# Kernel tuning notes

Measured on AMD Instinct MI355X. Metric: run time of the kernel, lower is better.

## Reference

```python
import jax, jax.numpy as jnp
import numpy as np

B, T, E, H = 8, 2048, 1024, 64

def setup_inputs() -> dict:
    key = jax.random.key(0)
    ks = jax.random.split(key, 7)
    s = 1.0 / np.sqrt(E)
    return {
        "x": jax.random.normal(ks[0], (B, T, E), dtype=jnp.float32),
        "Wq": jax.random.uniform(ks[1], (E, H), jnp.float32, -s, s),
        "bq": jax.random.uniform(ks[2], (H,), jnp.float32, -s, s),
        "Wk": jax.random.uniform(ks[3], (E, H), jnp.float32, -s, s),
        "bk": jax.random.uniform(ks[4], (H,), jnp.float32, -s, s),
        "Wv": jax.random.uniform(ks[5], (E, H), jnp.float32, -s, s),
        "bv": jax.random.uniform(ks[6], (H,), jnp.float32, -s, s),
        "mask": jnp.ones((B, T), dtype=jnp.int32),
    }

def reference(x, Wq, bq, Wk, bk, Wv, bv, mask):
    # QKV projections: [B,T,E] @ [E,H] -> [B,T,H]
    q = x @ Wq + bq
    k = x @ Wk + bk
    v = x @ Wv + bv
    scale = jnp.asarray(H, x.dtype) ** -0.5
    attn = jnp.einsum("bqh,bkh->bqk", q, k) * scale  # [B,T,T]
    pad = mask.astype(bool)[:, None, :]  # key padding mask broadcast over queries
    attn = jnp.where(pad, attn, jnp.asarray(-1e9, attn.dtype))
    attn = jax.nn.softmax(attn, axis=-1)
    # dropout p=0.0 (eval) -> identity
    return jnp.einsum("bqk,bkh->bqh", attn, v)
```

## Files before the change

### kernel.cpp

```cpp
#include <hip/hip_runtime.h>
#include <hip/hip_bf16.h>
#include <stdint.h>


typedef __attribute__((ext_vector_type(8))) short short8;
typedef __attribute__((ext_vector_type(4))) float floatx4;
typedef __attribute__((ext_vector_type(2))) uint32_t uint2v;
typedef __attribute__((ext_vector_type(4))) uint32_t uint4v;

static constexpr int Tn = 2048, En = 1024, Hn = 64;
static constexpr float kLog2e = 1.44269504088896340736f;

static __device__ __forceinline__ ushort f2bf(float f) {
  uint32_t u = __builtin_bit_cast(uint32_t, f);
  u += 0x7FFFu + ((u >> 16) & 1u);
  return (ushort)(u >> 16);
}
static __device__ __forceinline__ uint32_t cvt_pk(float lo, float hi) {
  uint32_t r;
  asm("v_cvt_pk_bf16_f32 %0, %1, %2" : "=v"(r) : "v"(lo), "v"(hi));
  return r;
}

__global__ __launch_bounds__(64) void k_packw(const float* __restrict__ Wq,
                                              const float* __restrict__ Wk,
                                              const float* __restrict__ Wv,
                                              ushort* __restrict__ wpack) {
  int blk = blockIdx.x;
  int kstep = blk / 12, ntile = blk % 12;
  int l = threadIdx.x;
  const float* W = (ntile < 4) ? Wq : (ntile < 8) ? Wk : Wv;
  int col = (ntile & 3) * 16 + (l & 15);
  int k0 = kstep * 32 + (l >> 4) * 8;
  short8 v;
#pragma unroll
  for (int j = 0; j < 8; ++j) v[j] = (short)f2bf(W[(k0 + j) * Hn + col]);
  *reinterpret_cast<short8*>(wpack + ((size_t)(kstep * 12 + ntile) * 64 + l) * 8) = v;
}

__global__ __launch_bounds__(256, 4) void k_qkv(const float* __restrict__ x,
                                                const ushort* __restrict__ wpack,
                                                const float* __restrict__ bq,
                                                const float* __restrict__ bk,
                                                const float* __restrict__ bv,
                                                ushort* __restrict__ q,
                                                ushort* __restrict__ k,
                                                ushort* __restrict__ vT2) {
  __shared__ float accS[2][64][28];
  int l = threadIdx.x & 63;
  int w = threadIdx.x >> 6;
  int ns = w & 1, ks2 = w >> 1;
  int n0 = ns * 6;
  int batch = blockIdx.x & 7;
  int chunk = blockIdx.x >> 3;
  int row0 = batch * Tn + chunk * 16;
  int lq = l & 15, g = l >> 4;
  const float* xrow = x + (size_t)(row0 + lq) * En + ks2 * 512 + g * 8;
  const ushort* wp = wpack + (size_t)l * 8;

  floatx4 acc[6];
#pragma unroll
  for (int n = 0; n < 6; ++n) acc[n] = (floatx4){0.f, 0.f, 0.f, 0.f};

  floatx4 xa[2][2];
  short8 bfr[2][6];
  xa[0][0] = *reinterpret_cast<const floatx4*>(xrow);
  xa[0][1] = *reinterpret_cast<const floatx4*>(xrow + 4);
  {
    int ks = ks2 * 16;
#pragma unroll
    for (int nn = 0; nn < 6; ++nn)
      bfr[0][nn] = *reinterpret_cast<const short8*>(wp + (size_t)(ks * 12 + n0 + nn) * 512);
  }

#pragma unroll
  for (int i = 0; i < 16; ++i) {
    const int cur = i & 1, nxt = cur ^ 1;
    if (i < 15) {
      xa[nxt][0] = *reinterpret_cast<const floatx4*>(xrow + (i + 1) * 32);
      xa[nxt][1] = *reinterpret_cast<const floatx4*>(xrow + (i + 1) * 32 + 4);
      int ksn = ks2 * 16 + i + 1;
#pragma unroll
      for (int nn = 0; nn < 6; ++nn)
        bfr[nxt][nn] = *reinterpret_cast<const short8*>(wp + (size_t)(ksn * 12 + n0 + nn) * 512);
    }
    uint4v aw;
    aw[0] = cvt_pk(xa[cur][0][0], xa[cur][0][1]);
    aw[1] = cvt_pk(xa[cur][0][2], xa[cur][0][3]);
    aw[2] = cvt_pk(xa[cur][1][0], xa[cur][1][1]);
    aw[3] = cvt_pk(xa[cur][1][2], xa[cur][1][3]);
    short8 af = __builtin_bit_cast(short8, aw);
#pragma unroll
    for (int nn = 0; nn < 6; ++nn)
      acc[nn] = __builtin_amdgcn_mfma_f32_16x16x32_bf16(af, bfr[cur][nn], acc[nn], 0, 0, 0);
  }

  if (ks2 == 1) {
#pragma unroll
    for (int nn = 0; nn < 6; ++nn)
      *reinterpret_cast<floatx4*>(&accS[ns][l][nn * 4]) = acc[nn];
  }
  __syncthreads();
  if (ks2 == 0) {
#pragma unroll
    for (int nn = 0; nn < 6; ++nn)
      acc[nn] += *reinterpret_cast<const floatx4*>(&accS[ns][l][nn * 4]);
#pragma unroll
    for (int nn = 0; nn < 6; ++nn) {
      int n = n0 + nn;
      int mat = n >> 2;
      int h = (n & 3) * 16 + lq;
      const float* bias = (mat == 0) ? bq : (mat == 1) ? bk : bv;
      float bias_f = bias[h];
      if (mat == 0) {
#pragma unroll
        for (int r = 0; r < 4; ++r)
          q[(size_t)(row0 + g * 4 + r) * Hn + h] = f2bf((acc[nn][r] + bias_f) * 0.125f);
      } else if (mat == 1) {
#pragma unroll
        for (int r = 0; r < 4; ++r)
          k[(size_t)(row0 + g * 4 + r) * Hn + h] = f2bf(acc[nn][r] + bias_f);
      } else {
        int tile = chunk >> 1;
        int off = (chunk & 1) * 16 + g * 4;
        uint2v pk;
        pk[0] = cvt_pk(acc[nn][0] + bias_f, acc[nn][1] + bias_f);
        pk[1] = cvt_pk(acc[nn][2] + bias_f, acc[nn][3] + bias_f);
        *reinterpret_cast<uint2v*>(vT2 + (((size_t)batch * 64 + tile) * 64 + h) * 32 + off) = pk;
      }
    }
  }
}

__global__ __launch_bounds__(512, 4) void k_attn(const ushort* __restrict__ qm,
                                                 const ushort* __restrict__ km,
                                                 const ushort* __restrict__ vT2,
                                                 const int* __restrict__ mask,
                                                 float* __restrict__ out) {
  __shared__ union SMem {
    ushort P[8][32 * 40];
    struct {
      float accS[4][64][36];
      float mS[4][2][64];
      float lS[4][2][64];
    } mg;
  } sm;

  int tid = threadIdx.x;
  int l = tid & 63, w = tid >> 6;
  int s = w;
  int bid = blockIdx.x;
  int b = bid & 7;
  int chunk = bid >> 3;
  int q0 = chunk * 32;
  int lq = l & 15, g = l >> 4;

  short8 qf[2][2];
#pragma unroll
  for (int qt2 = 0; qt2 < 2; ++qt2) {
    const ushort* qb = qm + ((size_t)(b * Tn + q0 + qt2 * 16 + lq)) * Hn + g * 8;
    qf[qt2][0] = *reinterpret_cast<const short8*>(qb);
    qf[qt2][1] = *reinterpret_cast<const short8*>(qb + 32);
  }

  const ushort* kp = km + ((size_t)(b * Tn + s * 256) + lq) * Hn + g * 8;
  const ushort* vp = vT2 + (((size_t)b * 64 + s * 8) * 64 + lq) * 32 + g * 8;

  const int* mrow = mask + b * Tn + s * 256 + l;
  unsigned long long bal64[4];
#pragma unroll
  for (int j = 0; j < 4; ++j) bal64[j] = __ballot(mrow[j * 64] != 0);

  ushort* Pw = &sm.P[w][0];
  uint32_t* Pw32 = reinterpret_cast<uint32_t*>(Pw);

  float m[2] = {-1e30f, -1e30f};
  float lsum[2] = {0.f, 0.f};
  floatx4 acc[2][4];
#pragma unroll
  for (int qt2 = 0; qt2 < 2; ++qt2)
#pragma unroll
    for (int mt = 0; mt < 4; ++mt) acc[qt2][mt] = (floatx4){0.f, 0.f, 0.f, 0.f};

  short8 kf[2][4];
#pragma unroll
  for (int t = 0; t < 2; ++t)
#pragma unroll
    for (int h = 0; h < 2; ++h)
      kf[0][t * 2 + h] = *reinterpret_cast<const short8*>(kp + t * 1024 + h * 32);

#pragma unroll
  for (int it = 0; it < 8; ++it) {
    const int cur = it & 1, nxt = cur ^ 1;
    if (it < 7) {
#pragma unroll
      for (int t = 0; t < 2; ++t)
#pragma unroll
        for (int h = 0; h < 2; ++h)
          kf[nxt][t * 2 + h] =
              *reinterpret_cast<const short8*>(kp + (it + 1) * 2048 + t * 1024 + h * 32);
    }
    short8 vf[4];
#pragma unroll
    for (int mt = 0; mt < 4; ++mt)
      vf[mt] = *reinterpret_cast<const short8*>(vp + it * 2048 + mt * 512);

    float sc[2][2][4];
#pragma unroll
    for (int qt2 = 0; qt2 < 2; ++qt2)
#pragma unroll
      for (int t = 0; t < 2; ++t) {
        floatx4 z = (floatx4){0.f, 0.f, 0.f, 0.f};
        z = __builtin_amdgcn_mfma_f32_16x16x32_bf16(kf[cur][t * 2 + 0], qf[qt2][0], z, 0, 0, 0);
        z = __builtin_amdgcn_mfma_f32_16x16x32_bf16(kf[cur][t * 2 + 1], qf[qt2][1], z, 0, 0, 0);
#pragma unroll
        for (int r = 0; r < 4; ++r) sc[qt2][t][r] = z[r];
      }
    unsigned int bal32 = (unsigned int)(bal64[it >> 1] >> ((it & 1) * 32));
    if (bal32 != 0xFFFFFFFFu) {
#pragma unroll
      for (int qt2 = 0; qt2 < 2; ++qt2)
#pragma unroll
        for (int t = 0; t < 2; ++t)
#pragma unroll
          for (int r = 0; r < 4; ++r)
            if (!((bal32 >> (t * 16 + g * 4 + r)) & 1u)) sc[qt2][t][r] = -1e9f;
    }
    float pmax0 = fmaxf(fmaxf(fmaxf(sc[0][0][0], sc[0][0][1]), fmaxf(sc[0][0][2], sc[0][0][3])),
                        fmaxf(fmaxf(sc[0][1][0], sc[0][1][1]), fmaxf(sc[0][1][2], sc[0][1][3])));
    float pmax1 = fmaxf(fmaxf(fmaxf(sc[1][0][0], sc[1][0][1]), fmaxf(sc[1][0][2], sc[1][0][3])),
                        fmaxf(fmaxf(sc[1][1][0], sc[1][1][1]), fmaxf(sc[1][1][2], sc[1][1][3])));
    if (!__all((pmax0 - m[0] <= 8.0f) && (pmax1 - m[1] <= 8.0f))) {
      float rm0 = fmaxf(pmax0, __shfl_xor(pmax0, 16));
      rm0 = fmaxf(rm0, __shfl_xor(rm0, 32));
      float rm1 = fmaxf(pmax1, __shfl_xor(pmax1, 16));
      rm1 = fmaxf(rm1, __shfl_xor(rm1, 32));
      float mn0 = fmaxf(m[0], rm0), mn1 = fmaxf(m[1], rm1);
      float a0 = __builtin_amdgcn_exp2f((m[0] - mn0) * kLog2e);
      float a1 = __builtin_amdgcn_exp2f((m[1] - mn1) * kLog2e);
      lsum[0] *= a0; lsum[1] *= a1;
#pragma unroll
      for (int mt = 0; mt < 4; ++mt) { acc[0][mt] *= a0; acc[1][mt] *= a1; }
      m[0] = mn0; m[1] = mn1;
    }
#pragma unroll
    for (int qt2 = 0; qt2 < 2; ++qt2) {
      float nmk = m[qt2] * kLog2e;
      float p[8];
#pragma unroll
      for (int t = 0; t < 2; ++t)
#pragma unroll
        for (int r = 0; r < 4; ++r)
          p[t * 4 + r] = __builtin_amdgcn_exp2f(__builtin_fmaf(sc[qt2][t][r], kLog2e, -nmk));
      lsum[qt2] += ((p[0] + p[1]) + (p[2] + p[3])) + ((p[4] + p[5]) + (p[6] + p[7]));
      uint2v pw0, pw1;
      pw0[0] = cvt_pk(p[0], p[1]); pw0[1] = cvt_pk(p[2], p[3]);
      pw1[0] = cvt_pk(p[4], p[5]); pw1[1] = cvt_pk(p[6], p[7]);
      int row = qt2 * 16 + lq;
      *reinterpret_cast<uint2v*>(Pw32 + row * 20 + g * 2) = pw0;
      *reinterpret_cast<uint2v*>(Pw32 + row * 20 + 8 + g * 2) = pw1;
    }
    short8 pf0 = *reinterpret_cast<const short8*>(Pw + (0 * 16 + lq) * 40 + g * 8);
    short8 pf1 = *reinterpret_cast<const short8*>(Pw + (1 * 16 + lq) * 40 + g * 8);
#pragma unroll
    for (int mt = 0; mt < 4; ++mt) {
      acc[0][mt] = __builtin_amdgcn_mfma_f32_16x16x32_bf16(vf[mt], pf0, acc[0][mt], 0, 0, 0);
      acc[1][mt] = __builtin_amdgcn_mfma_f32_16x16x32_bf16(vf[mt], pf1, acc[1][mt], 0, 0, 0);
    }
  }

#pragma unroll
  for (int qt2 = 0; qt2 < 2; ++qt2) {
    lsum[qt2] += __shfl_xor(lsum[qt2], 16);
    lsum[qt2] += __shfl_xor(lsum[qt2], 32);
  }

  __syncthreads();
  if (s >= 4) {
#pragma unroll
    for (int qt2 = 0; qt2 < 2; ++qt2) {
#pragma unroll
      for (int mt = 0; mt < 4; ++mt)
        *reinterpret_cast<floatx4*>(&sm.mg.accS[s - 4][l][qt2 * 16 + mt * 4]) = acc[qt2][mt];
      sm.mg.mS[s - 4][qt2][l] = m[qt2];
      sm.mg.lS[s - 4][qt2][l] = lsum[qt2];
    }
  }
  __syncthreads();
  if (s < 4) {
#pragma unroll
    for (int qt2 = 0; qt2 < 2; ++qt2) {
      float m2 = sm.mg.mS[s][qt2][l], l2 = sm.mg.lS[s][qt2][l];
      float mn = fmaxf(m[qt2], m2);
      float ea = __builtin_amdgcn_exp2f((m[qt2] - mn) * kLog2e);
      float eb = __builtin_amdgcn_exp2f((m2 - mn) * kLog2e);
      lsum[qt2] = lsum[qt2] * ea + l2 * eb;
#pragma unroll
      for (int mt = 0; mt < 4; ++mt) {
        floatx4 a = *reinterpret_cast<const floatx4*>(&sm.mg.accS[s][l][qt2 * 16 + mt * 4]);
#pragma unroll
        for (int r = 0; r < 4; ++r) acc[qt2][mt][r] = acc[qt2][mt][r] * ea + a[r] * eb;
      }
      m[qt2] = mn;
    }
  }
  __syncthreads();
  if (s >= 1 && s < 4) {
#pragma unroll
    for (int qt2 = 0; qt2 < 2; ++qt2) {
#pragma unroll
      for (int mt = 0; mt < 4; ++mt)
        *reinterpret_cast<floatx4*>(&sm.mg.accS[s - 1][l][qt2 * 16 + mt * 4]) = acc[qt2][mt];
      sm.mg.mS[s - 1][qt2][l] = m[qt2];
      sm.mg.lS[s - 1][qt2][l] = lsum[qt2];
    }
  }
  __syncthreads();
  if (s == 0) {
#pragma unroll
    for (int qt2 = 0; qt2 < 2; ++qt2) {
      float mtot = m[qt2];
#pragma unroll
      for (int si = 0; si < 3; ++si) mtot = fmaxf(mtot, sm.mg.mS[si][qt2][l]);
      float e0 = __builtin_amdgcn_exp2f((m[qt2] - mtot) * kLog2e);
      float ltot = lsum[qt2] * e0;
      float res[4][4];
#pragma unroll
      for (int mt = 0; mt < 4; ++mt)
#pragma unroll
        for (int r = 0; r < 4; ++r) res[mt][r] = acc[qt2][mt][r] * e0;
#pragma unroll
      for (int si = 0; si < 3; ++si) {
        float e = __builtin_amdgcn_exp2f((sm.mg.mS[si][qt2][l] - mtot) * kLog2e);
        ltot += sm.mg.lS[si][qt2][l] * e;
#pragma unroll
        for (int mt = 0; mt < 4; ++mt) {
          floatx4 a = *reinterpret_cast<const floatx4*>(&sm.mg.accS[si][l][qt2 * 16 + mt * 4]);
#pragma unroll
          for (int r = 0; r < 4; ++r) res[mt][r] += a[r] * e;
        }
      }
      float inv = 1.0f / ltot;
      float* obase = out + ((size_t)(b * Tn + q0 + qt2 * 16 + lq)) * Hn;
#pragma unroll
      for (int mt = 0; mt < 4; ++mt) {
        floatx4 o;
#pragma unroll
        for (int r = 0; r < 4; ++r) o[r] = res[mt][r] * inv;
        *reinterpret_cast<floatx4*>(obase + mt * 16 + g * 4) = o;
      }
    }
  }
}

extern "C" void kernel_launch(void* const* d_in, const int* in_sizes, int n_in,
                              void* d_out, int out_size, void* d_ws, size_t ws_size,
                              hipStream_t stream) {
  const float* x  = (const float*)d_in[0];
  const float* Wq = (const float*)d_in[1];
  const float* bq = (const float*)d_in[2];
  const float* Wk = (const float*)d_in[3];
  const float* bk = (const float*)d_in[4];
  const float* Wv = (const float*)d_in[5];
  const float* bv = (const float*)d_in[6];
  const int* mask = (const int*)d_in[7];
  float* outp = (float*)d_out;

  ushort* wpack = (ushort*)d_ws;
  ushort* qbuf  = wpack + 196608;
  ushort* kbuf  = qbuf + (size_t)16384 * 64;
  ushort* vT2   = kbuf + (size_t)16384 * 64;

  hipLaunchKernelGGL(k_packw, dim3(384), dim3(64), 0, stream, Wq, Wk, Wv, wpack);
  hipLaunchKernelGGL(k_qkv, dim3(1024), dim3(256), 0, stream, x, wpack, bq, bk, bv,
                     qbuf, kbuf, vT2);
  hipLaunchKernelGGL(k_attn, dim3(512), dim3(512), 0, stream, qbuf, kbuf, vT2, mask, outp);
}
```

Before: 69.34 us.

## Stage bf16 x tile in LDS and split QKV output tiles across waves

The QKV projection kernel now first converts the block's 16x1024 fp32 x rows to bf16 and stores them in shared memory. Each of the four waves then computes three full-K output tiles sequentially, reading A fragments from LDS. This replaces the split-K scheme with its register double-buffering and shared-memory reduction. The aim is to read x from global memory once per block instead of once per N-split wave pair, and to drop the reduction step. In exchange it gives up explicit prefetch pipelining and adds a serial load phase and about 33KB of LDS per block, which may reduce occupancy.

```diff
diff --git a/kernel.cpp b/kernel.cpp
--- a/kernel.cpp
+++ b/kernel.cpp
@@ -38,96 +38,70 @@
   *reinterpret_cast<short8*>(wpack + ((size_t)(kstep * 12 + ntile) * 64 + l) * 8) = v;
 }
 
-__global__ __launch_bounds__(256, 4) void k_qkv(const float* __restrict__ x,
-                                                const ushort* __restrict__ wpack,
-                                                const float* __restrict__ bq,
-                                                const float* __restrict__ bk,
-                                                const float* __restrict__ bv,
-                                                ushort* __restrict__ q,
-                                                ushort* __restrict__ k,
-                                                ushort* __restrict__ vT2) {
-  __shared__ float accS[2][64][28];
-  int l = threadIdx.x & 63;
-  int w = threadIdx.x >> 6;
-  int ns = w & 1, ks2 = w >> 1;
-  int n0 = ns * 6;
+__global__ __launch_bounds__(256) void k_qkv(const float* __restrict__ x,
+                                             const ushort* __restrict__ wpack,
+                                             const float* __restrict__ bq,
+                                             const float* __restrict__ bk,
+                                             const float* __restrict__ bv,
+                                             ushort* __restrict__ q,
+                                             ushort* __restrict__ k,
+                                             ushort* __restrict__ vT2) {
+  __shared__ ushort xs[16][1032];
+  int tid = threadIdx.x;
   int batch = blockIdx.x & 7;
   int chunk = blockIdx.x >> 3;
   int row0 = batch * Tn + chunk * 16;
+
+  {
+    int r = tid & 15;
+    int kc = tid >> 4;
+    const float* src = x + (size_t)(row0 + r) * En + kc * 64;
+    ushort* dst = &xs[r][kc * 64];
+#pragma unroll
+    for (int i = 0; i < 16; ++i) {
+      floatx4 f = *reinterpret_cast<const floatx4*>(src + i * 4);
+      uint2v u;
+      u[0] = cvt_pk(f[0], f[1]);
+      u[1] = cvt_pk(f[2], f[3]);
+      *reinterpret_cast<uint2v*>(dst + i * 4) = u;
+    }
+  }
+  __syncthreads();
+
+  int l = tid & 63;
+  int w = tid >> 6;
   int lq = l & 15, g = l >> 4;
-  const float* xrow = x + (size_t)(row0 + lq) * En + ks2 * 512 + g * 8;
-  const ushort* wp = wpack + (size_t)l * 8;
-
-  floatx4 acc[6];
-#pragma unroll
-  for (int n = 0; n < 6; ++n) acc[n] = (floatx4){0.f, 0.f, 0.f, 0.f};
-
-  floatx4 xa[2][2];
-  short8 bfr[2][6];
-  xa[0][0] = *reinterpret_cast<const floatx4*>(xrow);
-  xa[0][1] = *reinterpret_cast<const floatx4*>(xrow + 4);
-  {
-    int ks = ks2 * 16;
-#pragma unroll
-    for (int nn = 0; nn < 6; ++nn)
-      bfr[0][nn] = *reinterpret_cast<const short8*>(wp + (size_t)(ks * 12 + n0 + nn) * 512);
-  }
-
-#pragma unroll
-  for (int i = 0; i < 16; ++i) {
-    const int cur = i & 1, nxt = cur ^ 1;
-    if (i < 15) {
-      xa[nxt][0] = *reinterpret_cast<const floatx4*>(xrow + (i + 1) * 32);
-      xa[nxt][1] = *reinterpret_cast<const floatx4*>(xrow + (i + 1) * 32 + 4);
-      int ksn = ks2 * 16 + i + 1;
-#pragma unroll
-      for (int nn = 0; nn < 6; ++nn)
-        bfr[nxt][nn] = *reinterpret_cast<const short8*>(wp + (size_t)(ksn * 12 + n0 + nn) * 512);
-    }
-    uint4v aw;
-    aw[0] = cvt_pk(xa[cur][0][0], xa[cur][0][1]);
-    aw[1] = cvt_pk(xa[cur][0][2], xa[cur][0][3]);
-    aw[2] = cvt_pk(xa[cur][1][0], xa[cur][1][1]);
-    aw[3] = cvt_pk(xa[cur][1][2], xa[cur][1][3]);
-    short8 af = __builtin_bit_cast(short8, aw);
-#pragma unroll
-    for (int nn = 0; nn < 6; ++nn)
-      acc[nn] = __builtin_amdgcn_mfma_f32_16x16x32_bf16(af, bfr[cur][nn], acc[nn], 0, 0, 0);
-  }
-
-  if (ks2 == 1) {
-#pragma unroll
-    for (int nn = 0; nn < 6; ++nn)
-      *reinterpret_cast<floatx4*>(&accS[ns][l][nn * 4]) = acc[nn];
-  }
-  __syncthreads();
-  if (ks2 == 0) {
-#pragma unroll
-    for (int nn = 0; nn < 6; ++nn)
-      acc[nn] += *reinterpret_cast<const floatx4*>(&accS[ns][l][nn * 4]);
-#pragma unroll
-    for (int nn = 0; nn < 6; ++nn) {
-      int n = n0 + nn;
-      int mat = n >> 2;
-      int h = (n & 3) * 16 + lq;
-      const float* bias = (mat == 0) ? bq : (mat == 1) ? bk : bv;
-      float bias_f = bias[h];
-      if (mat == 0) {
-#pragma unroll
-        for (int r = 0; r < 4; ++r)
-          q[(size_t)(row0 + g * 4 + r) * Hn + h] = f2bf((acc[nn][r] + bias_f) * 0.125f);
-      } else if (mat == 1) {
-#pragma unroll
-        for (int r = 0; r < 4; ++r)
-          k[(size_t)(row0 + g * 4 + r) * Hn + h] = f2bf(acc[nn][r] + bias_f);
-      } else {
-        int tile = chunk >> 1;
-        int off = (chunk & 1) * 16 + g * 4;
-        uint2v pk;
-        pk[0] = cvt_pk(acc[nn][0] + bias_f, acc[nn][1] + bias_f);
-        pk[1] = cvt_pk(acc[nn][2] + bias_f, acc[nn][3] + bias_f);
-        *reinterpret_cast<uint2v*>(vT2 + (((size_t)batch * 64 + tile) * 64 + h) * 32 + off) = pk;
-      }
+
+#pragma unroll
+  for (int nn = 0; nn < 3; ++nn) {
+    int n = w * 3 + nn;
+    const ushort* wpn = wpack + ((size_t)n * 64 + l) * 8;
+    floatx4 acc = (floatx4){0.f, 0.f, 0.f, 0.f};
+#pragma unroll 4
+    for (int ks = 0; ks < 32; ++ks) {
+      short8 af = *reinterpret_cast<const short8*>(&xs[lq][ks * 32 + g * 8]);
+      short8 bf = *reinterpret_cast<const short8*>(wpn + (size_t)ks * 6144);
+      acc = __builtin_amdgcn_mfma_f32_16x16x32_bf16(af, bf, acc, 0, 0, 0);
+    }
+    int mat = n >> 2;
+    int h = (n & 3) * 16 + lq;
+    const float* bias = (mat == 0) ? bq : (mat == 1) ? bk : bv;
+    float bias_f = bias[h];
+    if (mat == 0) {
+#pragma unroll
+      for (int r = 0; r < 4; ++r)
+        q[(size_t)(row0 + g * 4 + r) * Hn + h] = f2bf((acc[r] + bias_f) * 0.125f);
+    } else if (mat == 1) {
+#pragma unroll
+      for (int r = 0; r < 4; ++r)
+        k[(size_t)(row0 + g * 4 + r) * Hn + h] = f2bf(acc[r] + bias_f);
+    } else {
+      int tile = chunk >> 1;
+      int off = (chunk & 1) * 16 + g * 4;
+      uint2v pk;
+      pk[0] = cvt_pk(acc[0] + bias_f, acc[1] + bias_f);
+      pk[1] = cvt_pk(acc[2] + bias_f, acc[3] + bias_f);
+      *reinterpret_cast<uint2v*>(vT2 + (((size_t)batch * 64 + tile) * 64 + h) * 32 + off) = pk;
     }
   }
 }
```

Result: faster. 65.08 us (-6.1%).

## Replace split-K reduction in QKV projection with per-wave row tiles

Applied to the files above, without the earlier changes.

The QKV projection kernel used to split the K dimension across wave pairs and merge their partial sums through shared memory behind a barrier. Each block now covers 32 rows, and each wave runs the full K=1024 loop for its own 16-row by 6-column tile, so the shared-memory reduction and __syncthreads go away. The grid shrinks from 1024 to 512 blocks and the occupancy hint is dropped. In exchange, each wave runs a serial chain twice as long, there are fewer blocks to hide latency, and each x row is read by two waves instead of one.

```diff
diff --git a/kernel.cpp b/kernel.cpp
--- a/kernel.cpp
+++ b/kernel.cpp
@@ -38,25 +38,24 @@
   *reinterpret_cast<short8*>(wpack + ((size_t)(kstep * 12 + ntile) * 64 + l) * 8) = v;
 }
 
-__global__ __launch_bounds__(256, 4) void k_qkv(const float* __restrict__ x,
-                                                const ushort* __restrict__ wpack,
-                                                const float* __restrict__ bq,
-                                                const float* __restrict__ bk,
-                                                const float* __restrict__ bv,
-                                                ushort* __restrict__ q,
-                                                ushort* __restrict__ k,
-                                                ushort* __restrict__ vT2) {
-  __shared__ float accS[2][64][28];
+__global__ __launch_bounds__(256) void k_qkv(const float* __restrict__ x,
+                                             const ushort* __restrict__ wpack,
+                                             const float* __restrict__ bq,
+                                             const float* __restrict__ bk,
+                                             const float* __restrict__ bv,
+                                             ushort* __restrict__ q,
+                                             ushort* __restrict__ k,
+                                             ushort* __restrict__ vT2) {
   int l = threadIdx.x & 63;
   int w = threadIdx.x >> 6;
-  int ns = w & 1, ks2 = w >> 1;
-  int n0 = ns * 6;
+  int rt = w & 1, ns = w >> 1;
   int batch = blockIdx.x & 7;
   int chunk = blockIdx.x >> 3;
-  int row0 = batch * Tn + chunk * 16;
+  int rl = chunk * 32 + rt * 16;
+  int row0 = batch * Tn + rl;
   int lq = l & 15, g = l >> 4;
-  const float* xrow = x + (size_t)(row0 + lq) * En + ks2 * 512 + g * 8;
-  const ushort* wp = wpack + (size_t)l * 8;
+  const float* xrow = x + (size_t)(row0 + lq) * En + g * 8;
+  const ushort* wpn = wpack + ((size_t)(ns * 6) * 64 + l) * 8;
 
   floatx4 acc[6];
 #pragma unroll
@@ -66,23 +65,20 @@
   short8 bfr[2][6];
   xa[0][0] = *reinterpret_cast<const floatx4*>(xrow);
   xa[0][1] = *reinterpret_cast<const floatx4*>(xrow + 4);
-  {
-    int ks = ks2 * 16;
-#pragma unroll
-    for (int nn = 0; nn < 6; ++nn)
-      bfr[0][nn] = *reinterpret_cast<const short8*>(wp + (size_t)(ks * 12 + n0 + nn) * 512);
-  }
-
-#pragma unroll
-  for (int i = 0; i < 16; ++i) {
+#pragma unroll
+  for (int nn = 0; nn < 6; ++nn)
+    bfr[0][nn] = *reinterpret_cast<const short8*>(wpn + (size_t)nn * 512);
+
+#pragma unroll
+  for (int i = 0; i < 32; ++i) {
     const int cur = i & 1, nxt = cur ^ 1;
-    if (i < 15) {
+    if (i < 31) {
       xa[nxt][0] = *reinterpret_cast<const floatx4*>(xrow + (i + 1) * 32);
       xa[nxt][1] = *reinterpret_cast<const floatx4*>(xrow + (i + 1) * 32 + 4);
-      int ksn = ks2 * 16 + i + 1;
 #pragma unroll
       for (int nn = 0; nn < 6; ++nn)
-        bfr[nxt][nn] = *reinterpret_cast<const short8*>(wp + (size_t)(ksn * 12 + n0 + nn) * 512);
+        bfr[nxt][nn] =
+            *reinterpret_cast<const short8*>(wpn + (size_t)(i + 1) * 6144 + nn * 512);
     }
     uint4v aw;
     aw[0] = cvt_pk(xa[cur][0][0], xa[cur][0][1]);
@@ -95,39 +91,28 @@
       acc[nn] = __builtin_amdgcn_mfma_f32_16x16x32_bf16(af, bfr[cur][nn], acc[nn], 0, 0, 0);
   }
 
-  if (ks2 == 1) {
-#pragma unroll
-    for (int nn = 0; nn < 6; ++nn)
-      *reinterpret_cast<floatx4*>(&accS[ns][l][nn * 4]) = acc[nn];
-  }
-  __syncthreads();
-  if (ks2 == 0) {
-#pragma unroll
-    for (int nn = 0; nn < 6; ++nn)
-      acc[nn] += *reinterpret_cast<const floatx4*>(&accS[ns][l][nn * 4]);
-#pragma unroll
-    for (int nn = 0; nn < 6; ++nn) {
-      int n = n0 + nn;
-      int mat = n >> 2;
-      int h = (n & 3) * 16 + lq;
-      const float* bias = (mat == 0) ? bq : (mat == 1) ? bk : bv;
-      float bias_f = bias[h];
-      if (mat == 0) {
-#pragma unroll
-        for (int r = 0; r < 4; ++r)
-          q[(size_t)(row0 + g * 4 + r) * Hn + h] = f2bf((acc[nn][r] + bias_f) * 0.125f);
-      } else if (mat == 1) {
-#pragma unroll
-        for (int r = 0; r < 4; ++r)
-          k[(size_t)(row0 + g * 4 + r) * Hn + h] = f2bf(acc[nn][r] + bias_f);
-      } else {
-        int tile = chunk >> 1;
-        int off = (chunk & 1) * 16 + g * 4;
-        uint2v pk;
-        pk[0] = cvt_pk(acc[nn][0] + bias_f, acc[nn][1] + bias_f);
-        pk[1] = cvt_pk(acc[nn][2] + bias_f, acc[nn][3] + bias_f);
-        *reinterpret_cast<uint2v*>(vT2 + (((size_t)batch * 64 + tile) * 64 + h) * 32 + off) = pk;
-      }
+  int tile = chunk;
+  int off = rt * 16 + g * 4;
+#pragma unroll
+  for (int nn = 0; nn < 6; ++nn) {
+    int n = ns * 6 + nn;
+    int mat = n >> 2;
+    int h = (n & 3) * 16 + lq;
+    const float* bias = (mat == 0) ? bq : (mat == 1) ? bk : bv;
+    float bias_f = bias[h];
+    if (mat == 0) {
+#pragma unroll
+      for (int r = 0; r < 4; ++r)
+        q[(size_t)(row0 + g * 4 + r) * Hn + h] = f2bf((acc[nn][r] + bias_f) * 0.125f);
+    } else if (mat == 1) {
+#pragma unroll
+      for (int r = 0; r < 4; ++r)
+        k[(size_t)(row0 + g * 4 + r) * Hn + h] = f2bf(acc[nn][r] + bias_f);
+    } else {
+      uint2v pk;
+      pk[0] = cvt_pk(acc[nn][0] + bias_f, acc[nn][1] + bias_f);
+      pk[1] = cvt_pk(acc[nn][2] + bias_f, acc[nn][3] + bias_f);
+      *reinterpret_cast<uint2v*>(vT2 + (((size_t)batch * 64 + tile) * 64 + h) * 32 + off) = pk;
     }
   }
 }
@@ -372,7 +357,7 @@
   ushort* vT2   = kbuf + (size_t)16384 * 64;
 
   hipLaunchKernelGGL(k_packw, dim3(384), dim3(64), 0, stream, Wq, Wk, Wv, wpack);
-  hipLaunchKernelGGL(k_qkv, dim3(1024), dim3(256), 0, stream, x, wpack, bq, bk, bv,
+  hipLaunchKernelGGL(k_qkv, dim3(512), dim3(256), 0, stream, x, wpack, bq, bk, bv,
                      qbuf, kbuf, vT2);
   hipLaunchKernelGGL(k_attn, dim3(512), dim3(512), 0, stream, qbuf, kbuf, vT2, mask, outp);
 }
```

After: 68.84 us. No clear change (-0.7%).
